# Kernel tuning notes

Measured on AMD Instinct MI355X. Metric: run time of the kernel, lower is better.

## Reference

```python
import jax, jax.numpy as jnp
import numpy as np

B, K, L, H = 64, 32, 64, 256


def setup_inputs() -> dict:
    key = jax.random.key(0)
    ks = jax.random.split(key, 24)
    def rnd(i, shape, scale):
        return jax.random.normal(ks[i], shape, dtype=jnp.float32) * scale
    s = 0.05  # small init for weights to keep activations sane
    return {
        'h_ue': rnd(0, (B, K, H), 1.0),
        'h_ap': rnd(1, (B, L, H), 1.0),
        'e':    rnd(2, (B, L * K, H), 1.0),
        # msg_ap_to_ue: Linear(2H->H), Linear(H->H)
        'a2u_w1': rnd(3, (H, 2 * H), s), 'a2u_b1': rnd(4, (H,), s),
        'a2u_w2': rnd(5, (H, H), s),     'a2u_b2': rnd(6, (H,), s),
        # msg_ue_to_ap
        'u2a_w1': rnd(7, (H, 2 * H), s), 'u2a_b1': rnd(8, (H,), s),
        'u2a_w2': rnd(9, (H, H), s),     'u2a_b2': rnd(10, (H,), s),
        # GRUCell (PyTorch layout: weight_ih (3H,H), weight_hh (3H,H))
        'ue_wih': rnd(11, (3 * H, H), s), 'ue_bih': rnd(12, (3 * H,), s),
        'ue_whh': rnd(13, (3 * H, H), s), 'ue_bhh': rnd(14, (3 * H,), s),
        'ap_wih': rnd(15, (3 * H, H), s), 'ap_bih': rnd(16, (3 * H,), s),
        'ap_whh': rnd(17, (3 * H, H), s), 'ap_bhh': rnd(18, (3 * H,), s),
        # edge_update: Linear(3H->H), Linear(H->H)
        'ed_w1': rnd(19, (H, 3 * H), s), 'ed_b1': rnd(20, (H,), s),
        'ed_w2': rnd(21, (H, H), s),     'ed_b2': rnd(22, (H,), s),
    }


def _gru(x, h, wih, bih, whh, bhh):
    # PyTorch GRUCell semantics
    gi = jnp.einsum('...h,oh->...o', x, wih) + bih
    gh = jnp.einsum('...h,oh->...o', h, whh) + bhh
    i_r, i_z, i_n = jnp.split(gi, 3, axis=-1)
    h_r, h_z, h_n = jnp.split(gh, 3, axis=-1)
    r = jax.nn.sigmoid(i_r + h_r)
    z = jax.nn.sigmoid(i_z + h_z)
    n = jnp.tanh(i_n + r * h_n)
    return (1.0 - z) * n + z * h


def reference(h_ue, h_ap, e,
              a2u_w1, a2u_b1, a2u_w2, a2u_b2,
              u2a_w1, u2a_b1, u2a_w2, u2a_b2,
              ue_wih, ue_bih, ue_whh, ue_bhh,
              ap_wih, ap_bih, ap_whh, ap_bhh,
              ed_w1, ed_b1, ed_w2, ed_b2):
    Bd, Kd, Hd = h_ue.shape
    Ld = h_ap.shape[1]
    e4 = e.reshape(Bd, Ld, Kd, Hd)  # edge (b, l, k) on dense bipartite graph

    # --- AP -> UE messages: MLP(concat[h_ap_src, e]); split first linear ---
    pre = (jnp.einsum('blh,oh->blo', h_ap, a2u_w1[:, :Hd])[:, :, None, :]
           + jnp.einsum('blkh,oh->blko', e4, a2u_w1[:, Hd:]) + a2u_b1)
    msg = jnp.einsum('blkh,oh->blko', jax.nn.relu(pre), a2u_w2) + a2u_b2
    m_ue = msg.mean(axis=1)  # mean over AP neighbors -> (B,K,H)

    # --- UE -> AP messages ---
    pre = (jnp.einsum('bkh,oh->bko', h_ue, u2a_w1[:, :Hd])[:, None, :, :]
           + jnp.einsum('blkh,oh->blko', e4, u2a_w1[:, Hd:]) + u2a_b1)
    msg = jnp.einsum('blkh,oh->blko', jax.nn.relu(pre), u2a_w2) + u2a_b2
    m_ap = msg.mean(axis=2)  # mean over UE neighbors -> (B,L,H)

    # --- GRU node updates ---
    h_ue_new = _gru(m_ue, h_ue, ue_wih, ue_bih, ue_whh, ue_bhh)
    h_ap_new = _gru(m_ap, h_ap, ap_wih, ap_bih, ap_whh, ap_bhh)

    # --- edge update: MLP(concat[src=UE_new, dst=AP_new, e]) ---
    pre = (jnp.einsum('bkh,oh->bko', h_ue_new, ed_w1[:, :Hd])[:, None, :, :]
           + jnp.einsum('blh,oh->blo', h_ap_new, ed_w1[:, Hd:2 * Hd])[:, :, None, :]
           + jnp.einsum('blkh,oh->blko', e4, ed_w1[:, 2 * Hd:]) + ed_b1)
    e_new = jnp.einsum('blkh,oh->blko', jax.nn.relu(pre), ed_w2) + ed_b2

    return h_ue_new, h_ap_new, e_new.reshape(Bd, Ld * Kd, Hd)
```

## Files before the change

kernel.cpp:

```cpp
#include <hip/hip_runtime.h>

#define HH 256
#define BB 64
#define KK 32
#define LL 64
#define LGRP 8

typedef __bf16 bf16_t;
typedef __attribute__((ext_vector_type(8))) __bf16 bf16x8;
typedef __attribute__((ext_vector_type(4))) float f32x4;

__device__ __forceinline__ bf16x8 ld_a8(const float* __restrict__ p) {
  const f32x4* q = (const f32x4*)p;
  f32x4 a = q[0], b = q[1];
  bf16x8 r;
  r[0] = (__bf16)a[0]; r[1] = (__bf16)a[1]; r[2] = (__bf16)a[2]; r[3] = (__bf16)a[3];
  r[4] = (__bf16)b[0]; r[5] = (__bf16)b[1]; r[6] = (__bf16)b[2]; r[7] = (__bf16)b[3];
  return r;
}

__device__ __forceinline__ void ld_tile(const float* __restrict__ E, int tid, f32x4 r[4]) {
  const f32x4* q = (const f32x4*)(E + tid * 16);
  r[0] = q[0]; r[1] = q[1]; r[2] = q[2]; r[3] = q[3];
}
__device__ __forceinline__ void wr_tile(bf16_t* buf, int tid, const f32x4 r[4]) {
  int row = tid >> 4;
  int colb = (tid & 15) * 32;
  bf16x8 v0, v1;
  v0[0] = (__bf16)r[0][0]; v0[1] = (__bf16)r[0][1]; v0[2] = (__bf16)r[0][2]; v0[3] = (__bf16)r[0][3];
  v0[4] = (__bf16)r[1][0]; v0[5] = (__bf16)r[1][1]; v0[6] = (__bf16)r[1][2]; v0[7] = (__bf16)r[1][3];
  v1[0] = (__bf16)r[2][0]; v1[1] = (__bf16)r[2][1]; v1[2] = (__bf16)r[2][2]; v1[3] = (__bf16)r[2][3];
  v1[4] = (__bf16)r[3][0]; v1[5] = (__bf16)r[3][1]; v1[6] = (__bf16)r[3][2]; v1[7] = (__bf16)r[3][3];
  int swz = (row & 7) << 4;
  *(bf16x8*)((char*)buf + row * 512 + (colb ^ swz)) = v0;
  *(bf16x8*)((char*)buf + row * 512 + ((colb + 16) ^ swz)) = v1;
}

template<int LDB>
__device__ __forceinline__ void mm_f32A(const float* __restrict__ A,
                                        const bf16_t* __restrict__ B,
                                        f32x4 acc[2][4], int lane) {
  const int c = lane & 15, g = lane >> 4;
#pragma unroll
  for (int ks = 0; ks < 8; ++ks) {
    const int ko = ks * 32 + g * 8;
    bf16x8 a0 = ld_a8(A + (size_t)c * HH + ko);
    bf16x8 a1 = ld_a8(A + (size_t)(16 + c) * HH + ko);
#pragma unroll
    for (int nt = 0; nt < 4; ++nt) {
      bf16x8 bb = *(const bf16x8*)(B + (size_t)(nt * 16 + c) * LDB + ko);
      acc[0][nt] = __builtin_amdgcn_mfma_f32_16x16x32_bf16(a0, bb, acc[0][nt], 0, 0, 0);
      acc[1][nt] = __builtin_amdgcn_mfma_f32_16x16x32_bf16(a1, bb, acc[1][nt], 0, 0, 0);
    }
  }
}

__global__ __launch_bounds__(256) void prep_kernel(
    const float* w0, const float* w1, const float* w2, const float* w3,
    const float* w4, const float* w5, const float* w6, const float* w7,
    const float* w8, const float* w9, bf16_t* wb) {
  int i = blockIdx.x * 256 + threadIdx.x;
  const float* s; int o; float sc = 1.f;
  if      (i < 131072)  { s = w0; o = i; }
  else if (i < 196608)  { s = w1; o = i - 131072; sc = 1.f / 64.f; }
  else if (i < 327680)  { s = w2; o = i - 196608; }
  else if (i < 393216)  { s = w3; o = i - 327680; sc = 1.f / 32.f; }
  else if (i < 589824)  { s = w4; o = i - 393216; }
  else if (i < 786432)  { s = w5; o = i - 589824; }
  else if (i < 983040)  { s = w6; o = i - 786432; }
  else if (i < 1179648) { s = w7; o = i - 983040; }
  else if (i < 1376256) { s = w8; o = i - 1179648; }
  else                  { s = w9; o = i - 1376256; }
  wb[i] = (__bf16)(s[o] * sc);
}

template<int LDW>
__global__ __launch_bounds__(256) void proj2_kernel(
    const float* __restrict__ X0, const bf16_t* __restrict__ W0,
    const float* __restrict__ b0, float* __restrict__ out0, int n0,
    const float* __restrict__ X1, const bf16_t* __restrict__ W1,
    const float* __restrict__ b1, float* __restrict__ out1) {
  const int blk = blockIdx.x;
  const float* X; const bf16_t* W; const float* bias; float* out; int row0;
  if (blk < n0) { X = X0; W = W0; bias = b0; out = out0; row0 = blk * 32; }
  else          { X = X1; W = W1; bias = b1; out = out1; row0 = (blk - n0) * 32; }
  const int tid = threadIdx.x, w = tid >> 6, lane = tid & 63;
  const int colw = w * 64, c = lane & 15, g = lane >> 4;
  f32x4 acc[2][4];
#pragma unroll
  for (int nt = 0; nt < 4; ++nt) {
    float bv = bias ? bias[colw + nt * 16 + c] : 0.f;
    f32x4 t = {bv, bv, bv, bv};
    acc[0][nt] = t; acc[1][nt] = t;
  }
  mm_f32A<LDW>(X + (size_t)row0 * HH, W + (size_t)colw * LDW, acc, lane);
#pragma unroll
  for (int m = 0; m < 2; ++m)
#pragma unroll
    for (int nt = 0; nt < 4; ++nt)
#pragma unroll
      for (int rr = 0; rr < 4; ++rr) {
        int row = row0 + m * 16 + g * 4 + rr;
        out[(size_t)row * HH + colw + nt * 16 + c] = acc[m][nt][rr];
      }
}

__global__ __launch_bounds__(512) void phaseA_kernel(
    const float* __restrict__ e, const float* __restrict__ p_ap,
    const float* __restrict__ p_ue,
    const bf16_t* __restrict__ wu1e, const bf16_t* __restrict__ wa1e,
    float* __restrict__ part, float* __restrict__ R_ap) {
  __shared__ bf16_t ebuf[2][32 * 256];
  const int blk = blockIdx.x;
  const int b = blk >> 3, lc = blk & 7;
  const int tid = threadIdx.x, w = tid >> 6, lane = tid & 63;
  const int colw = w * 32, c = lane & 15, g = lane >> 4;
  const int l0 = lc * LGRP;

  bf16x8 wU[2][8], wA[2][8];
#pragma unroll
  for (int nt = 0; nt < 2; ++nt)
#pragma unroll
    for (int ks = 0; ks < 8; ++ks) {
      size_t off = (size_t)(colw + nt * 16 + c) * 512 + ks * 32 + g * 8;
      wU[nt][ks] = *(const bf16x8*)(wu1e + off);
      wA[nt][ks] = *(const bf16x8*)(wa1e + off);
    }

  float pue[2][2][4];
#pragma unroll
  for (int m = 0; m < 2; ++m)
#pragma unroll
    for (int nt = 0; nt < 2; ++nt)
#pragma unroll
      for (int rr = 0; rr < 4; ++rr)
        pue[m][nt][rr] = p_ue[(size_t)(b * KK + m * 16 + g * 4 + rr) * HH + colw + nt * 16 + c];

  f32x4 accU[2][2];
  const f32x4 z4 = {0.f, 0.f, 0.f, 0.f};
#pragma unroll
  for (int m = 0; m < 2; ++m)
#pragma unroll
    for (int nt = 0; nt < 2; ++nt) accU[m][nt] = z4;

  f32x4 rs[4];
  ld_tile(e + (size_t)((b * LL + l0) * KK) * HH, tid, rs);
  wr_tile(ebuf[0], tid, rs);

  for (int li = 0; li < LGRP; ++li) {
    __syncthreads();
    const int l = l0 + li;
    if (li + 1 < LGRP) ld_tile(e + (size_t)((b * LL + l + 1) * KK) * HH, tid, rs);

    f32x4 aU[2][2], aA[2][2];
#pragma unroll
    for (int nt = 0; nt < 2; ++nt) {
      float pa = p_ap[(size_t)(b * LL + l) * HH + colw + nt * 16 + c];
      f32x4 t = {pa, pa, pa, pa};
      aA[0][nt] = t; aA[1][nt] = t;
#pragma unroll
      for (int rr = 0; rr < 4; ++rr) {
        aU[0][nt][rr] = pue[0][nt][rr];
        aU[1][nt][rr] = pue[1][nt][rr];
      }
    }
    const bf16_t* eb = ebuf[li & 1];
    const int swz = (c & 7) << 4;
#pragma unroll
    for (int ks = 0; ks < 8; ++ks) {
      const int kb = (ks * 32 + g * 8) * 2;
      bf16x8 a0 = *(const bf16x8*)((const char*)eb + c * 512 + (kb ^ swz));
      bf16x8 a1 = *(const bf16x8*)((const char*)eb + (16 + c) * 512 + (kb ^ swz));
#pragma unroll
      for (int nt = 0; nt < 2; ++nt) {
        aU[0][nt] = __builtin_amdgcn_mfma_f32_16x16x32_bf16(a0, wU[nt][ks], aU[0][nt], 0, 0, 0);
        aU[1][nt] = __builtin_amdgcn_mfma_f32_16x16x32_bf16(a1, wU[nt][ks], aU[1][nt], 0, 0, 0);
        aA[0][nt] = __builtin_amdgcn_mfma_f32_16x16x32_bf16(a0, wA[nt][ks], aA[0][nt], 0, 0, 0);
        aA[1][nt] = __builtin_amdgcn_mfma_f32_16x16x32_bf16(a1, wA[nt][ks], aA[1][nt], 0, 0, 0);
      }
    }

#pragma unroll
    for (int nt = 0; nt < 2; ++nt) {
      float s = 0.f;
#pragma unroll
      for (int m = 0; m < 2; ++m)
#pragma unroll
        for (int rr = 0; rr < 4; ++rr) s += fmaxf(aU[m][nt][rr], 0.f);
      s += __shfl_xor(s, 16);
      s += __shfl_xor(s, 32);
      if (lane < 16)
        R_ap[(size_t)(b * LL + l) * HH + colw + nt * 16 + lane] = s;
    }
#pragma unroll
    for (int m = 0; m < 2; ++m)
#pragma unroll
      for (int nt = 0; nt < 2; ++nt)
#pragma unroll
        for (int rr = 0; rr < 4; ++rr)
          accU[m][nt][rr] += fmaxf(aA[m][nt][rr], 0.f);

    if (li + 1 < LGRP) wr_tile(ebuf[(li + 1) & 1], tid, rs);
  }

#pragma unroll
  for (int m = 0; m < 2; ++m)
#pragma unroll
    for (int nt = 0; nt < 2; ++nt)
#pragma unroll
      for (int rr = 0; rr < 4; ++rr) {
        int krow = m * 16 + g * 4 + rr;
        part[(size_t)((lc * BB + b) * KK + krow) * HH + colw + nt * 16 + c] = accU[m][nt][rr];
      }
}

__global__ __launch_bounds__(256) void reduce_kernel(
    const float* __restrict__ part, float* __restrict__ R_ue) {
  int i = blockIdx.x * 256 + threadIdx.x;
  float s = 0.f;
#pragma unroll
  for (int lc = 0; lc < 8; ++lc) s += part[(size_t)lc * 524288 + i];
  R_ue[i] = s;
}

__global__ __launch_bounds__(256) void gru_kernel(
    const float* __restrict__ m_ue, const float* __restrict__ h_ue,
    const bf16_t* __restrict__ wih_ue, const bf16_t* __restrict__ whh_ue,
    const float* __restrict__ ue_bih, const float* __restrict__ ue_bhh,
    float* __restrict__ hue_new,
    const float* __restrict__ m_ap, const float* __restrict__ h_ap,
    const bf16_t* __restrict__ wih_ap, const bf16_t* __restrict__ whh_ap,
    const float* __restrict__ ap_bih, const float* __restrict__ ap_bhh,
    float* __restrict__ hap_new) {
  const int blk = blockIdx.x;
  const float *x, *h, *bih, *bhh; const bf16_t *wih, *whh; float* hout; int row0;
  if (blk < 64) { x = m_ue; h = h_ue; wih = wih_ue; whh = whh_ue;
                  bih = ue_bih; bhh = ue_bhh; hout = hue_new; row0 = blk * 32; }
  else          { x = m_ap; h = h_ap; wih = wih_ap; whh = whh_ap;
                  bih = ap_bih; bhh = ap_bhh; hout = hap_new; row0 = (blk - 64) * 32; }
  const int tid = threadIdx.x, w = tid >> 6, lane = tid & 63;
  const int colw = w * 64, c = lane & 15, g = lane >> 4;
  f32x4 aR[2][4], aZ[2][4], aN[2][4], aHN[2][4];
#pragma unroll
  for (int nt = 0; nt < 4; ++nt) {
    int col = colw + nt * 16 + c;
    float vR = bih[col] + bhh[col];
    float vZ = bih[256 + col] + bhh[256 + col];
    float vN = bih[512 + col];
    float vH = bhh[512 + col];
    f32x4 tR = {vR, vR, vR, vR}, tZ = {vZ, vZ, vZ, vZ};
    f32x4 tN = {vN, vN, vN, vN}, tH = {vH, vH, vH, vH};
    aR[0][nt] = tR; aR[1][nt] = tR;
    aZ[0][nt] = tZ; aZ[1][nt] = tZ;
    aN[0][nt] = tN; aN[1][nt] = tN;
    aHN[0][nt] = tH; aHN[1][nt] = tH;
  }
  const float* X = x + (size_t)row0 * HH;
  const float* Hp = h + (size_t)row0 * HH;
  mm_f32A<256>(X,  wih + (size_t)(0   + colw) * 256, aR, lane);
  mm_f32A<256>(Hp, whh + (size_t)(0   + colw) * 256, aR, lane);
  mm_f32A<256>(X,  wih + (size_t)(256 + colw) * 256, aZ, lane);
  mm_f32A<256>(Hp, whh + (size_t)(256 + colw) * 256, aZ, lane);
  mm_f32A<256>(X,  wih + (size_t)(512 + colw) * 256, aN, lane);
  mm_f32A<256>(Hp, whh + (size_t)(512 + colw) * 256, aHN, lane);
#pragma unroll
  for (int m = 0; m < 2; ++m)
#pragma unroll
    for (int nt = 0; nt < 4; ++nt)
#pragma unroll
      for (int rr = 0; rr < 4; ++rr) {
        int row = row0 + m * 16 + g * 4 + rr;
        int col = colw + nt * 16 + c;
        float rg = 1.f / (1.f + __expf(-aR[m][nt][rr]));
        float zg = 1.f / (1.f + __expf(-aZ[m][nt][rr]));
        float t = aN[m][nt][rr] + rg * aHN[m][nt][rr];
        t = fminf(fmaxf(t, -15.f), 15.f);
        float ex = __expf(-2.f * t);
        float ng = (1.f - ex) / (1.f + ex);
        float ho = h[(size_t)row * HH + col];
        hout[(size_t)row * HH + col] = (1.f - zg) * ng + zg * ho;
      }
}

__global__ __launch_bounds__(512) void phaseC_kernel(
    const float* __restrict__ e, const float* __restrict__ q_ue,
    const float* __restrict__ q_ap,
    const bf16_t* __restrict__ wed1e, const bf16_t* __restrict__ wed2,
    const float* __restrict__ ed_b2, float* __restrict__ e_new) {
  __shared__ bf16_t ebuf[2][32 * 256];
  __shared__ bf16_t pbuf[32 * 256];
  const int blk = blockIdx.x;
  const int b = blk >> 3, lc = blk & 7;
  const int tid = threadIdx.x, w = tid >> 6, lane = tid & 63;
  const int colw = w * 32, c = lane & 15, g = lane >> 4;
  const int l0 = lc * LGRP;

  bf16x8 w1[2][8], w2[2][8];
#pragma unroll
  for (int nt = 0; nt < 2; ++nt)
#pragma unroll
    for (int ks = 0; ks < 8; ++ks) {
      w1[nt][ks] = *(const bf16x8*)(wed1e + (size_t)(colw + nt * 16 + c) * 768 + ks * 32 + g * 8);
      w2[nt][ks] = *(const bf16x8*)(wed2  + (size_t)(colw + nt * 16 + c) * 256 + ks * 32 + g * 8);
    }

  float qU[2][2][4];
#pragma unroll
  for (int m = 0; m < 2; ++m)
#pragma unroll
    for (int nt = 0; nt < 2; ++nt)
#pragma unroll
      for (int rr = 0; rr < 4; ++rr)
        qU[m][nt][rr] = q_ue[(size_t)(b * KK + m * 16 + g * 4 + rr) * HH + colw + nt * 16 + c];
  float b2v[2];
#pragma unroll
  for (int nt = 0; nt < 2; ++nt) b2v[nt] = ed_b2[colw + nt * 16 + c];

  f32x4 rs[4];
  ld_tile(e + (size_t)((b * LL + l0) * KK) * HH, tid, rs);
  wr_tile(ebuf[0], tid, rs);

  for (int li = 0; li < LGRP; ++li) {
    __syncthreads();
    const int l = l0 + li;

    f32x4 a1[2][2];
#pragma unroll
    for (int nt = 0; nt < 2; ++nt) {
      float qa = q_ap[(size_t)(b * LL + l) * HH + colw + nt * 16 + c];
#pragma unroll
      for (int rr = 0; rr < 4; ++rr) {
        a1[0][nt][rr] = qa + qU[0][nt][rr];
        a1[1][nt][rr] = qa + qU[1][nt][rr];
      }
    }
    const bf16_t* eb = ebuf[li & 1];
    const int swz = (c & 7) << 4;
#pragma unroll
    for (int ks = 0; ks < 8; ++ks) {
      const int kb = (ks * 32 + g * 8) * 2;
      bf16x8 a0 = *(const bf16x8*)((const char*)eb + c * 512 + (kb ^ swz));
      bf16x8 a1f = *(const bf16x8*)((const char*)eb + (16 + c) * 512 + (kb ^ swz));
#pragma unroll
      for (int nt = 0; nt < 2; ++nt) {
        a1[0][nt] = __builtin_amdgcn_mfma_f32_16x16x32_bf16(a0,  w1[nt][ks], a1[0][nt], 0, 0, 0);
        a1[1][nt] = __builtin_amdgcn_mfma_f32_16x16x32_bf16(a1f, w1[nt][ks], a1[1][nt], 0, 0, 0);
      }
    }
    if (li + 1 < LGRP) ld_tile(e + (size_t)((b * LL + l + 1) * KK) * HH, tid, rs);

#pragma unroll
    for (int m = 0; m < 2; ++m)
#pragma unroll
      for (int nt = 0; nt < 2; ++nt)
#pragma unroll
        for (int rr = 0; rr < 4; ++rr) {
          int row = m * 16 + g * 4 + rr;
          int col = colw + nt * 16 + c;
          float v = fmaxf(a1[m][nt][rr], 0.f);
          int off = row * 512 + ((col * 2) ^ ((row & 7) << 4));
          *(bf16_t*)((char*)pbuf + off) = (__bf16)v;
        }
    __syncthreads();

    f32x4 a2[2][2];
#pragma unroll
    for (int nt = 0; nt < 2; ++nt) {
      f32x4 t = {b2v[nt], b2v[nt], b2v[nt], b2v[nt]};
      a2[0][nt] = t; a2[1][nt] = t;
    }
#pragma unroll
    for (int ks = 0; ks < 8; ++ks) {
      const int kb = (ks * 32 + g * 8) * 2;
      bf16x8 a0 = *(const bf16x8*)((const char*)pbuf + c * 512 + (kb ^ swz));
      bf16x8 a1f = *(const bf16x8*)((const char*)pbuf + (16 + c) * 512 + (kb ^ swz));
#pragma unroll
      for (int nt = 0; nt < 2; ++nt) {
        a2[0][nt] = __builtin_amdgcn_mfma_f32_16x16x32_bf16(a0,  w2[nt][ks], a2[0][nt], 0, 0, 0);
        a2[1][nt] = __builtin_amdgcn_mfma_f32_16x16x32_bf16(a1f, w2[nt][ks], a2[1][nt], 0, 0, 0);
      }
    }
#pragma unroll
    for (int m = 0; m < 2; ++m)
#pragma unroll
      for (int nt = 0; nt < 2; ++nt)
#pragma unroll
        for (int rr = 0; rr < 4; ++rr) {
          int row = m * 16 + g * 4 + rr;
          int col = colw + nt * 16 + c;
          e_new[(size_t)((b * LL + l) * KK + row) * HH + col] = a2[m][nt][rr];
        }
    if (li + 1 < LGRP) wr_tile(ebuf[(li + 1) & 1], tid, rs);
  }
}

extern "C" void kernel_launch(void* const* d_in, const int* in_sizes, int n_in,
                              void* d_out, int out_size, void* d_ws, size_t ws_size,
                              hipStream_t stream) {
  const float* h_ue   = (const float*)d_in[0];
  const float* h_ap   = (const float*)d_in[1];
  const float* e      = (const float*)d_in[2];
  const float* a2u_w1 = (const float*)d_in[3];
  const float* a2u_b1 = (const float*)d_in[4];
  const float* a2u_w2 = (const float*)d_in[5];
  const float* a2u_b2 = (const float*)d_in[6];
  const float* u2a_w1 = (const float*)d_in[7];
  const float* u2a_b1 = (const float*)d_in[8];
  const float* u2a_w2 = (const float*)d_in[9];
  const float* u2a_b2 = (const float*)d_in[10];
  const float* ue_wih = (const float*)d_in[11];
  const float* ue_bih = (const float*)d_in[12];
  const float* ue_whh = (const float*)d_in[13];
  const float* ue_bhh = (const float*)d_in[14];
  const float* ap_wih = (const float*)d_in[15];
  const float* ap_bih = (const float*)d_in[16];
  const float* ap_whh = (const float*)d_in[17];
  const float* ap_bhh = (const float*)d_in[18];
  const float* ed_w1  = (const float*)d_in[19];
  const float* ed_b1  = (const float*)d_in[20];
  const float* ed_w2  = (const float*)d_in[21];
  const float* ed_b2  = (const float*)d_in[22];

  bf16_t* wb      = (bf16_t*)d_ws;
  bf16_t* wa1     = wb;
  bf16_t* wa2s    = wa1 + 131072;
  bf16_t* wu1     = wa2s + 65536;
  bf16_t* wu2s    = wu1 + 131072;
  bf16_t* wih_ue  = wu2s + 65536;
  bf16_t* whh_ue  = wih_ue + 196608;
  bf16_t* wih_ap  = whh_ue + 196608;
  bf16_t* whh_ap  = wih_ap + 196608;
  bf16_t* wed1    = whh_ap + 196608;
  bf16_t* wed2    = wed1 + 196608;
  float* fbase = (float*)((char*)d_ws + 2883584);
  float* m_ue = fbase;
  float* m_ap = m_ue + 524288;
  float* p_ap = m_ap + 1048576;
  float* p_ue = p_ap + 1048576;
  float* q_ue = p_ue + 524288;
  float* q_ap = q_ue + 524288;
  float* part = q_ap + 1048576;
  float* R_ue = q_ue;
  float* R_ap = q_ap;

  float* out      = (float*)d_out;
  float* hue_new  = out;
  float* hap_new  = out + 524288;
  float* e_new    = out + 1572864;

  prep_kernel<<<5632, 256, 0, stream>>>(a2u_w1, a2u_w2, u2a_w1, u2a_w2,
                                        ue_wih, ue_whh, ap_wih, ap_whh,
                                        ed_w1, ed_w2, wb);
  proj2_kernel<512><<<192, 256, 0, stream>>>(h_ap, wa1, a2u_b1, p_ap, 128,
                                             h_ue, wu1, u2a_b1, p_ue);
  phaseA_kernel<<<512, 512, 0, stream>>>(e, p_ap, p_ue, wu1 + 256, wa1 + 256,
                                         part, R_ap);
  reduce_kernel<<<2048, 256, 0, stream>>>(part, R_ue);
  proj2_kernel<256><<<192, 256, 0, stream>>>(R_ue, wa2s, a2u_b2, m_ue, 64,
                                             R_ap, wu2s, u2a_b2, m_ap);
  gru_kernel<<<192, 256, 0, stream>>>(m_ue, h_ue, wih_ue, whh_ue, ue_bih, ue_bhh, hue_new,
                                      m_ap, h_ap, wih_ap, whh_ap, ap_bih, ap_bhh, hap_new);
  proj2_kernel<768><<<192, 256, 0, stream>>>(hue_new, wed1, ed_b1, q_ue, 64,
                                             hap_new, wed1 + 256, nullptr, q_ap);
  phaseC_kernel<<<512, 512, 0, stream>>>(e, q_ue, q_ap, wed1 + 512, wed2, ed_b2, e_new);
}
```

Measured before the change: 215.8 us.

## Software-pipeline phaseC edge MLP to remove a barrier per iteration

Double-buffers the hidden-activation shared buffer and skews the loop so the second GEMM for the previous l runs in the same iteration as the first GEMM for the current l. This drops one __syncthreads per iteration and issues the next edge tile's global load earlier, so more of its latency is hidden. The cost is an extra 16KB of LDS per block, which may lower occupancy, plus an epilogue that handles the last l separately.

```diff
diff --git a/kernel.cpp b/kernel.cpp
--- a/kernel.cpp
+++ b/kernel.cpp
@@ -288,7 +288,7 @@
     const bf16_t* __restrict__ wed1e, const bf16_t* __restrict__ wed2,
     const float* __restrict__ ed_b2, float* __restrict__ e_new) {
   __shared__ bf16_t ebuf[2][32 * 256];
-  __shared__ bf16_t pbuf[32 * 256];
+  __shared__ bf16_t pbuf[2][32 * 256];
   const int blk = blockIdx.x;
   const int b = blk >> 3, lc = blk & 7;
   const int tid = threadIdx.x, w = tid >> 6, lane = tid & 63;
@@ -316,6 +316,8 @@
 #pragma unroll
   for (int nt = 0; nt < 2; ++nt) b2v[nt] = ed_b2[colw + nt * 16 + c];
 
+  const int swz = (c & 7) << 4;
+
   f32x4 rs[4];
   ld_tile(e + (size_t)((b * LL + l0) * KK) * HH, tid, rs);
   wr_tile(ebuf[0], tid, rs);
@@ -323,6 +325,38 @@
   for (int li = 0; li < LGRP; ++li) {
     __syncthreads();
     const int l = l0 + li;
+    if (li + 1 < LGRP) ld_tile(e + (size_t)((b * LL + l + 1) * KK) * HH, tid, rs);
+
+    if (li > 0) {
+      const bf16_t* pb = pbuf[(li - 1) & 1];
+      f32x4 a2[2][2];
+#pragma unroll
+      for (int nt = 0; nt < 2; ++nt) {
+        f32x4 t = {b2v[nt], b2v[nt], b2v[nt], b2v[nt]};
+        a2[0][nt] = t; a2[1][nt] = t;
+      }
+#pragma unroll
+      for (int ks = 0; ks < 8; ++ks) {
+        const int kb = (ks * 32 + g * 8) * 2;
+        bf16x8 a0 = *(const bf16x8*)((const char*)pb + c * 512 + (kb ^ swz));
+        bf16x8 a1f = *(const bf16x8*)((const char*)pb + (16 + c) * 512 + (kb ^ swz));
+#pragma unroll
+        for (int nt = 0; nt < 2; ++nt) {
+          a2[0][nt] = __builtin_amdgcn_mfma_f32_16x16x32_bf16(a0,  w2[nt][ks], a2[0][nt], 0, 0, 0);
+          a2[1][nt] = __builtin_amdgcn_mfma_f32_16x16x32_bf16(a1f, w2[nt][ks], a2[1][nt], 0, 0, 0);
+        }
+      }
+#pragma unroll
+      for (int m = 0; m < 2; ++m)
+#pragma unroll
+        for (int nt = 0; nt < 2; ++nt)
+#pragma unroll
+          for (int rr = 0; rr < 4; ++rr) {
+            int row = m * 16 + g * 4 + rr;
+            int col = colw + nt * 16 + c;
+            e_new[(size_t)((b * LL + l - 1) * KK + row) * HH + col] = a2[m][nt][rr];
+          }
+    }
 
     f32x4 a1[2][2];
 #pragma unroll
@@ -335,7 +369,6 @@
       }
     }
     const bf16_t* eb = ebuf[li & 1];
-    const int swz = (c & 7) << 4;
 #pragma unroll
     for (int ks = 0; ks < 8; ++ks) {
       const int kb = (ks * 32 + g * 8) * 2;
@@ -347,8 +380,7 @@
         a1[1][nt] = __builtin_amdgcn_mfma_f32_16x16x32_bf16(a1f, w1[nt][ks], a1[1][nt], 0, 0, 0);
       }
     }
-    if (li + 1 < LGRP) ld_tile(e + (size_t)((b * LL + l + 1) * KK) * HH, tid, rs);
-
+    bf16_t* pw = pbuf[li & 1];
 #pragma unroll
     for (int m = 0; m < 2; ++m)
 #pragma unroll
@@ -359,10 +391,15 @@
           int col = colw + nt * 16 + c;
           float v = fmaxf(a1[m][nt][rr], 0.f);
           int off = row * 512 + ((col * 2) ^ ((row & 7) << 4));
-          *(bf16_t*)((char*)pbuf + off) = (__bf16)v;
+          *(bf16_t*)((char*)pw + off) = (__bf16)v;
         }
-    __syncthreads();
-
+
+    if (li + 1 < LGRP) wr_tile(ebuf[(li + 1) & 1], tid, rs);
+  }
+
+  __syncthreads();
+  {
+    const bf16_t* pb = pbuf[(LGRP - 1) & 1];
     f32x4 a2[2][2];
 #pragma unroll
     for (int nt = 0; nt < 2; ++nt) {
@@ -372,8 +409,8 @@
 #pragma unroll
     for (int ks = 0; ks < 8; ++ks) {
       const int kb = (ks * 32 + g * 8) * 2;
-      bf16x8 a0 = *(const bf16x8*)((const char*)pbuf + c * 512 + (kb ^ swz));
-      bf16x8 a1f = *(const bf16x8*)((const char*)pbuf + (16 + c) * 512 + (kb ^ swz));
+      bf16x8 a0 = *(const bf16x8*)((const char*)pb + c * 512 + (kb ^ swz));
+      bf16x8 a1f = *(const bf16x8*)((const char*)pb + (16 + c) * 512 + (kb ^ swz));
 #pragma unroll
       for (int nt = 0; nt < 2; ++nt) {
         a2[0][nt] = __builtin_amdgcn_mfma_f32_16x16x32_bf16(a0,  w2[nt][ks], a2[0][nt], 0, 0, 0);
@@ -388,9 +425,8 @@
         for (int rr = 0; rr < 4; ++rr) {
           int row = m * 16 + g * 4 + rr;
           int col = colw + nt * 16 + c;
-          e_new[(size_t)((b * LL + l) * KK + row) * HH + col] = a2[m][nt][rr];
+          e_new[(size_t)((b * LL + l0 + LGRP - 1) * KK + row) * HH + col] = a2[m][nt][rr];
         }
-    if (li + 1 < LGRP) wr_tile(ebuf[(li + 1) & 1], tid, rs);
   }
 }
 
```

Measured after the change: 214.7 us. No clear change (-0.5%).
